# Performance work log

Measured on AMD Instinct MI355X. Metric: run time of the kernel, lower is better.

The kernel has to match this reference:

```python
import jax, jax.numpy as jnp
import numpy as np
import math

DIM = 256
D_STATE = 16
D_CONV = 4
EXPAND = 2
D_INNER = EXPAND * DIM
DT_RANK = math.ceil(DIM / 16)
B_, H_, W_ = 2, 48, 48


def setup_inputs() -> dict:
    key = jax.random.key(0)
    ks = jax.random.split(key, 13)
    s = lambda *sh: 1.0 / np.sqrt(sh[-1])
    inp = {
        "x": jax.random.normal(ks[0], (B_, DIM, H_, W_), jnp.float32),
        "ln_w": jnp.ones((DIM,), jnp.float32),
        "ln_b": jnp.zeros((DIM,), jnp.float32),
        "in_proj_w": jax.random.normal(ks[1], (2 * D_INNER, DIM), jnp.float32) * s(DIM),
        "conv_w": jax.random.normal(ks[2], (D_INNER, 1, D_CONV), jnp.float32) * s(D_CONV),
        "conv_b": jax.random.normal(ks[3], (D_INNER,), jnp.float32) * 0.1,
        "x_proj_w": jax.random.normal(ks[4], (DT_RANK + 2 * D_STATE, D_INNER), jnp.float32) * s(D_INNER),
        "dt_proj_w": jax.random.normal(ks[5], (D_INNER, DT_RANK), jnp.float32) * s(DT_RANK),
        "dt_proj_b": jax.random.uniform(ks[6], (D_INNER,), jnp.float32, -4.0, -1.0),  # softplus -> small dt
        "A_log": jnp.log(jnp.broadcast_to(jnp.arange(1, D_STATE + 1, dtype=jnp.float32), (D_INNER, D_STATE))),
        "D": jnp.ones((D_INNER,), jnp.float32),
        "out_proj_w": jax.random.normal(ks[7], (DIM, D_INNER), jnp.float32) * s(D_INNER),
        "gamma": jax.random.normal(ks[8], (1,), jnp.float32) * 0.1,
    }
    return inp


def _mamba(seq, in_proj_w, conv_w, conv_b, x_proj_w, dt_proj_w, dt_proj_b, A_log, D, out_proj_w):
    # seq: [B, L, dim]
    B, L, _ = seq.shape
    xz = seq @ in_proj_w.T                       # [B, L, 2*d_inner]
    x_in, z = jnp.split(xz, 2, axis=-1)
    # depthwise causal conv over time
    xt = jnp.transpose(x_in, (0, 2, 1))          # [B, d_inner, L]
    xc = jax.lax.conv_general_dilated(
        xt, conv_w, window_strides=(1,), padding=[(D_CONV - 1, 0)],
        feature_group_count=D_INNER, dimension_numbers=("NCH", "OIH", "NCH"))
    xc = xc + conv_b[None, :, None]
    xc = jax.nn.silu(xc)
    xu = jnp.transpose(xc, (0, 2, 1))            # [B, L, d_inner]
    # input-dependent SSM params
    x_dbl = xu @ x_proj_w.T                      # [B, L, dt_rank + 2N]
    dt, Bm, Cm = jnp.split(x_dbl, [DT_RANK, DT_RANK + D_STATE], axis=-1)
    delta = jax.nn.softplus(dt @ dt_proj_w.T + dt_proj_b)   # [B, L, d_inner]
    A = -jnp.exp(A_log)                          # [d_inner, N]
    dA = jnp.exp(delta[..., None] * A)           # [B, L, d_inner, N]
    dBx = (delta * xu)[..., None] * Bm[:, :, None, :]        # [B, L, d_inner, N]

    def step(h, ins):
        dA_t, dBx_t, C_t = ins
        h = dA_t * h + dBx_t                     # [B, d_inner, N]
        y = jnp.einsum("bdn,bn->bd", h, C_t)
        return h, y

    h0 = jnp.zeros((B, D_INNER, D_STATE), seq.dtype)
    xs = (jnp.swapaxes(dA, 0, 1), jnp.swapaxes(dBx, 0, 1), jnp.swapaxes(Cm, 0, 1))
    _, ys = jax.lax.scan(step, h0, xs)           # ys: [L, B, d_inner]
    y = jnp.swapaxes(ys, 0, 1) + xu * D          # [B, L, d_inner]
    y = y * jax.nn.silu(z)
    return y @ out_proj_w.T                      # [B, L, dim]


def reference(x, ln_w, ln_b, in_proj_w, conv_w, conv_b, x_proj_w, dt_proj_w,
              dt_proj_b, A_log, D, out_proj_w, gamma):
    B, C, H, W = x.shape
    shortcut = x
    xp = jnp.transpose(x, (0, 2, 3, 1))          # [B, H, W, C]
    mu = jnp.mean(xp, axis=-1, keepdims=True)
    var = jnp.var(xp, axis=-1, keepdims=True)
    xn = (xp - mu) * jax.lax.rsqrt(var + 1e-5) * ln_w + ln_b
    seq = xn.reshape(B, H * W, C)
    y = _mamba(seq, in_proj_w, conv_w, conv_b, x_proj_w, dt_proj_w, dt_proj_b,
               A_log, D, out_proj_w)
    y = jnp.transpose(y.reshape(B, H, W, C), (0, 3, 1, 2))
    return shortcut + gamma * y
```

## Files before the change

kernel.cpp:

```cpp
#include <hip/hip_runtime.h>
#include <math.h>

#define DIMC 256
#define DST 16
#define DIN 512
#define BB 2
#define HH 48
#define WW 48
#define LL (HH*WW)
#define MM (BB*LL)
#define CH 24
#define NC 96
#define NGRP (BB*DIN)
#define NSEQ (NGRP*DST)

typedef unsigned short ushort_t;
typedef __attribute__((ext_vector_type(8))) short bf16x8;
typedef __attribute__((ext_vector_type(4))) float f32x4;

__device__ __forceinline__ float silu_f(float a){ return a / (1.f + expf(-a)); }
__device__ __forceinline__ float softplus_f(float a){ return a > 20.f ? a : log1pf(__expf(a)); }
__device__ __forceinline__ ushort_t f2bf(float f) {
    unsigned u = __float_as_uint(f);
    u += 0x7FFFu + ((u >> 16) & 1u);
    return (ushort_t)(u >> 16);
}
__device__ __forceinline__ float bf2f(ushort_t h) {
    return __uint_as_float(((unsigned)h) << 16);
}

__global__ __launch_bounds__(256) void ln_kernel(const float* __restrict__ x,
    const float* __restrict__ w, const float* __restrict__ bgain,
    ushort_t* __restrict__ xn) {
    int pos = blockIdx.x;
    int b = pos / LL, l = pos % LL;
    int c = threadIdx.x;
    float v = x[((size_t)b*DIMC + c)*LL + l];
    float s = v, s2 = v*v;
    #pragma unroll
    for (int o = 32; o; o >>= 1) { s += __shfl_down(s, o); s2 += __shfl_down(s2, o); }
    __shared__ float ss[4], ss2[4];
    int wid = c >> 6;
    if ((c & 63) == 0) { ss[wid] = s; ss2[wid] = s2; }
    __syncthreads();
    float tot  = ss[0]+ss[1]+ss[2]+ss[3];
    float tot2 = ss2[0]+ss2[1]+ss2[2]+ss2[3];
    float mu = tot * (1.f/DIMC);
    float var = tot2 * (1.f/DIMC) - mu*mu;
    float r = rsqrtf(var + 1e-5f);
    xn[(size_t)pos*DIMC + c] = f2bf((v - mu)*r*w[c] + bgain[c]);
}

#define W0N (1024*256)
#define W1N (48*512)
#define W2N (256*512)
__global__ __launch_bounds__(256) void wconv_kernel(const float* __restrict__ w0,
    const float* __restrict__ w1, const float* __restrict__ w2,
    ushort_t* __restrict__ o0, ushort_t* __restrict__ o1, ushort_t* __restrict__ o2) {
    int i = blockIdx.x * 256 + threadIdx.x;
    if (i < W0N) o0[i] = f2bf(w0[i]);
    else if (i < W0N + W1N) o1[i - W0N] = f2bf(w1[i - W0N]);
    else o2[i - W0N - W1N] = f2bf(w2[i - W0N - W1N]);
}

template<int EPI>
__global__ __launch_bounds__(256) void mfma_gemm(const ushort_t* __restrict__ A,
    const ushort_t* __restrict__ W, float* __restrict__ C, int M, int N, int K,
    const float* __restrict__ Xres, const float* __restrict__ gammap,
    float* __restrict__ Out) {
    __shared__ ushort_t Asl[64][72];
    __shared__ ushort_t Bsl[64][72];
    int tid = threadIdx.x;
    int bm = blockIdx.y * 64;
    int bn = blockIdx.x * 64;
    int w = tid >> 6, l = tid & 63;
    int wr = (w >> 1) * 32, wc = (w & 1) * 32;
    int fr = l & 15, fg = l >> 4;
    f32x4 acc[2][2] = {};
    for (int k0 = 0; k0 < K; k0 += 64) {
        #pragma unroll
        for (int s = 0; s < 2; s++) {
            int c = tid + s*256;
            int r = c >> 3, c8 = (c & 7) * 8;
            *(uint4*)&Asl[r][c8] = *(const uint4*)(A + (size_t)(bm + r)*K + k0 + c8);
            uint4 wv = make_uint4(0u,0u,0u,0u);
            if (bn + r < N) wv = *(const uint4*)(W + (size_t)(bn + r)*K + k0 + c8);
            *(uint4*)&Bsl[r][c8] = wv;
        }
        __syncthreads();
        #pragma unroll
        for (int kk = 0; kk < 2; kk++) {
            int ko = kk*32 + fg*8;
            bf16x8 a0 = *(const bf16x8*)&Asl[wr + fr][ko];
            bf16x8 a1 = *(const bf16x8*)&Asl[wr + 16 + fr][ko];
            bf16x8 b0 = *(const bf16x8*)&Bsl[wc + fr][ko];
            bf16x8 b1 = *(const bf16x8*)&Bsl[wc + 16 + fr][ko];
            acc[0][0] = __builtin_amdgcn_mfma_f32_16x16x32_bf16(a0, b0, acc[0][0], 0,0,0);
            acc[0][1] = __builtin_amdgcn_mfma_f32_16x16x32_bf16(a0, b1, acc[0][1], 0,0,0);
            acc[1][0] = __builtin_amdgcn_mfma_f32_16x16x32_bf16(a1, b0, acc[1][0], 0,0,0);
            acc[1][1] = __builtin_amdgcn_mfma_f32_16x16x32_bf16(a1, b1, acc[1][1], 0,0,0);
        }
        __syncthreads();
    }
    if (EPI == 0) {
        #pragma unroll
        for (int mi = 0; mi < 2; mi++)
            #pragma unroll
            for (int nj = 0; nj < 2; nj++) {
                int n = bn + wc + nj*16 + fr;
                if (n < N) {
                    int mbase = bm + wr + mi*16 + fg*4;
                    #pragma unroll
                    for (int i = 0; i < 4; i++)
                        C[(size_t)(mbase + i)*N + n] = acc[mi][nj][i];
                }
            }
    } else {
        float g = gammap[0];
        int b = (bm >= LL) ? 1 : 0;
        #pragma unroll
        for (int mi = 0; mi < 2; mi++)
            #pragma unroll
            for (int nj = 0; nj < 2; nj++) {
                int n = bn + wc + nj*16 + fr;
                int mbase = bm + wr + mi*16 + fg*4;
                #pragma unroll
                for (int i = 0; i < 4; i++) {
                    size_t o = ((size_t)(b*DIMC + n))*LL + (size_t)(mbase + i - b*LL);
                    Out[o] = fmaf(g, acc[mi][nj][i], Xres[o]);
                }
            }
    }
}

__global__ __launch_bounds__(256) void conv_kernel(const float* __restrict__ xz,
    const float* __restrict__ cw, const float* __restrict__ cb,
    ushort_t* __restrict__ xu) {
    int idx = blockIdx.x * 256 + threadIdx.x;
    int d = idx & (DIN-1);
    int ml = idx >> 9;
    int l = ml % LL;
    float acc = cb[d];
    #pragma unroll
    for (int j = 0; j < 4; j++) {
        int ll = l - 3 + j;
        if (ll >= 0) acc = fmaf(cw[d*4 + j], xz[(size_t)(ml - l + ll)*1024 + d], acc);
    }
    xu[(size_t)ml*DIN + d] = f2bf(silu_f(acc));
}

#define LOAD16(arr, p) { float4 q0=(p)[0],q1=(p)[1],q2=(p)[2],q3=(p)[3]; \
    arr[0]=q0.x;arr[1]=q0.y;arr[2]=q0.z;arr[3]=q0.w; arr[4]=q1.x;arr[5]=q1.y;arr[6]=q1.z;arr[7]=q1.w; \
    arr[8]=q2.x;arr[9]=q2.y;arr[10]=q2.z;arr[11]=q2.w; arr[12]=q3.x;arr[13]=q3.y;arr[14]=q3.z;arr[15]=q3.w; }

__global__ __launch_bounds__(256) void scan_phase1(
    const ushort_t* __restrict__ xu, const float* __restrict__ xdbl,
    const float* __restrict__ dtw, const float* __restrict__ dtb,
    const float* __restrict__ A_log,
    float* __restrict__ aprod, float* __restrict__ hend) {
    int t = blockIdx.x * 256 + threadIdx.x;
    int g = t & (NGRP-1);
    int c = t >> 10;
    int b = g >> 9, d = g & (DIN-1);
    float dw[16], A[16], h[16], a[16];
    LOAD16(dw, (const float4*)(dtw + (size_t)d*16));
    #pragma unroll
    for (int n = 0; n < 16; n++) A[n] = -__expf(A_log[d*DST + n]);
    #pragma unroll
    for (int n = 0; n < 16; n++) { h[n] = 0.f; a[n] = 1.f; }
    float bias = dtb[d];
    int m0 = b*LL + c*CH;
    for (int l = 0; l < CH; l++) {
        int m = m0 + l;
        const float4* xr = (const float4*)(xdbl + (size_t)m*48);
        float4 t0 = xr[0], t1 = xr[1], t2 = xr[2], t3 = xr[3];
        float dlt = bias;
        dlt=fmaf(t0.x,dw[0],dlt); dlt=fmaf(t0.y,dw[1],dlt); dlt=fmaf(t0.z,dw[2],dlt); dlt=fmaf(t0.w,dw[3],dlt);
        dlt=fmaf(t1.x,dw[4],dlt); dlt=fmaf(t1.y,dw[5],dlt); dlt=fmaf(t1.z,dw[6],dlt); dlt=fmaf(t1.w,dw[7],dlt);
        dlt=fmaf(t2.x,dw[8],dlt); dlt=fmaf(t2.y,dw[9],dlt); dlt=fmaf(t2.z,dw[10],dlt); dlt=fmaf(t2.w,dw[11],dlt);
        dlt=fmaf(t3.x,dw[12],dlt); dlt=fmaf(t3.y,dw[13],dlt); dlt=fmaf(t3.z,dw[14],dlt); dlt=fmaf(t3.w,dw[15],dlt);
        dlt = softplus_f(dlt);
        float xv = bf2f(xu[(size_t)m*DIN + d]);
        float dbx = dlt * xv;
        float Bv[16];
        LOAD16(Bv, xr + 4);
        #pragma unroll
        for (int n = 0; n < 16; n++) {
            float dA = __expf(dlt * A[n]);
            h[n] = fmaf(dA, h[n], dbx * Bv[n]);
            a[n] *= dA;
        }
    }
    float4* ap = (float4*)(aprod + ((size_t)c*NGRP + g)*16);
    float4* hp = (float4*)(hend  + ((size_t)c*NGRP + g)*16);
    ap[0] = make_float4(a[0],a[1],a[2],a[3]);   ap[1] = make_float4(a[4],a[5],a[6],a[7]);
    ap[2] = make_float4(a[8],a[9],a[10],a[11]); ap[3] = make_float4(a[12],a[13],a[14],a[15]);
    hp[0] = make_float4(h[0],h[1],h[2],h[3]);   hp[1] = make_float4(h[4],h[5],h[6],h[7]);
    hp[2] = make_float4(h[8],h[9],h[10],h[11]); hp[3] = make_float4(h[12],h[13],h[14],h[15]);
}

__global__ __launch_bounds__(256) void scan_phase2(const float* __restrict__ aprod,
    const float* __restrict__ hend, float* __restrict__ hin) {
    int u = blockIdx.x * 256 + threadIdx.x;
    float h = 0.f;
    #pragma unroll 4
    for (int c = 0; c < NC; c++) {
        size_t ci = (size_t)c*NSEQ + u;
        hin[ci] = h;
        h = fmaf(aprod[ci], h, hend[ci]);
    }
}

__global__ __launch_bounds__(256) void scan_phase3(
    const ushort_t* __restrict__ xu, const float* __restrict__ xdbl,
    const float* __restrict__ dtw, const float* __restrict__ dtb,
    const float* __restrict__ A_log, const float* __restrict__ Dp,
    const float* __restrict__ xz, const float* __restrict__ hin,
    ushort_t* __restrict__ yg) {
    int t = blockIdx.x * 256 + threadIdx.x;
    int g = t & (NGRP-1);
    int c = t >> 10;
    int b = g >> 9, d = g & (DIN-1);
    float dw[16], A[16], h[16];
    LOAD16(dw, (const float4*)(dtw + (size_t)d*16));
    #pragma unroll
    for (int n = 0; n < 16; n++) A[n] = -__expf(A_log[d*DST + n]);
    LOAD16(h, (const float4*)(hin + ((size_t)c*NGRP + g)*16));
    float bias = dtb[d];
    float Dd = Dp[d];
    int m0 = b*LL + c*CH;
    for (int l = 0; l < CH; l++) {
        int m = m0 + l;
        const float4* xr = (const float4*)(xdbl + (size_t)m*48);
        float4 t0 = xr[0], t1 = xr[1], t2 = xr[2], t3 = xr[3];
        float dlt = bias;
        dlt=fmaf(t0.x,dw[0],dlt); dlt=fmaf(t0.y,dw[1],dlt); dlt=fmaf(t0.z,dw[2],dlt); dlt=fmaf(t0.w,dw[3],dlt);
        dlt=fmaf(t1.x,dw[4],dlt); dlt=fmaf(t1.y,dw[5],dlt); dlt=fmaf(t1.z,dw[6],dlt); dlt=fmaf(t1.w,dw[7],dlt);
        dlt=fmaf(t2.x,dw[8],dlt); dlt=fmaf(t2.y,dw[9],dlt); dlt=fmaf(t2.z,dw[10],dlt); dlt=fmaf(t2.w,dw[11],dlt);
        dlt=fmaf(t3.x,dw[12],dlt); dlt=fmaf(t3.y,dw[13],dlt); dlt=fmaf(t3.z,dw[14],dlt); dlt=fmaf(t3.w,dw[15],dlt);
        dlt = softplus_f(dlt);
        float xv = bf2f(xu[(size_t)m*DIN + d]);
        float dbx = dlt * xv;
        float Bv[16], Cv[16];
        LOAD16(Bv, xr + 4);
        LOAD16(Cv, xr + 8);
        float y = 0.f;
        #pragma unroll
        for (int n = 0; n < 16; n++) {
            float dA = __expf(dlt * A[n]);
            h[n] = fmaf(dA, h[n], dbx * Bv[n]);
            y = fmaf(h[n], Cv[n], y);
        }
        float z = xz[(size_t)m*1024 + 512 + d];
        float yv = fmaf(xv, Dd, y);
        yg[(size_t)m*DIN + d] = f2bf(yv * (z / (1.f + __expf(-z))));
    }
}

extern "C" void kernel_launch(void* const* d_in, const int* in_sizes, int n_in,
                              void* d_out, int out_size, void* d_ws, size_t ws_size,
                              hipStream_t stream) {
    const float* x         = (const float*)d_in[0];
    const float* ln_w      = (const float*)d_in[1];
    const float* ln_b      = (const float*)d_in[2];
    const float* in_proj_w = (const float*)d_in[3];
    const float* conv_w    = (const float*)d_in[4];
    const float* conv_b    = (const float*)d_in[5];
    const float* x_proj_w  = (const float*)d_in[6];
    const float* dt_proj_w = (const float*)d_in[7];
    const float* dt_proj_b = (const float*)d_in[8];
    const float* A_log     = (const float*)d_in[9];
    const float* Dp        = (const float*)d_in[10];
    const float* out_proj_w= (const float*)d_in[11];
    const float* gamma     = (const float*)d_in[12];
    float* out = (float*)d_out;

    float* ws = (float*)d_ws;
    float* xz    = ws;
    float* x_dbl = xz    + (size_t)MM*1024;
    float* aprod = x_dbl + (size_t)MM*48;
    float* hend  = aprod + (size_t)NC*NSEQ;
    float* hin   = hend  + (size_t)NC*NSEQ;
    ushort_t* xn  = (ushort_t*)(hin + (size_t)NC*NSEQ);
    ushort_t* xu  = xn  + (size_t)MM*DIMC;
    ushort_t* yg  = xu  + (size_t)MM*DIN;
    ushort_t* win = yg  + (size_t)MM*DIN;
    ushort_t* wxp = win + (size_t)W0N;
    ushort_t* wout= wxp + (size_t)W1N;

    ln_kernel<<<MM, 256, 0, stream>>>(x, ln_w, ln_b, xn);
    wconv_kernel<<<(W0N+W1N+W2N)/256, 256, 0, stream>>>(in_proj_w, x_proj_w, out_proj_w, win, wxp, wout);
    mfma_gemm<0><<<dim3(1024/64, MM/64), 256, 0, stream>>>(xn, win, xz, MM, 1024, DIMC, nullptr, nullptr, nullptr);
    conv_kernel<<<(MM*DIN)/256, 256, 0, stream>>>(xz, conv_w, conv_b, xu);
    mfma_gemm<0><<<dim3(1, MM/64), 256, 0, stream>>>(xu, wxp, x_dbl, MM, 48, DIN, nullptr, nullptr, nullptr);
    scan_phase1<<<(NC*NGRP)/256, 256, 0, stream>>>(xu, x_dbl, dt_proj_w, dt_proj_b, A_log, aprod, hend);
    scan_phase2<<<NSEQ/256, 256, 0, stream>>>(aprod, hend, hin);
    scan_phase3<<<(NC*NGRP)/256, 256, 0, stream>>>(xu, x_dbl, dt_proj_w, dt_proj_b, A_log, Dp, xz, hin, yg);
    mfma_gemm<2><<<dim3(DIMC/64, MM/64), 256, 0, stream>>>(yg, wout, nullptr, MM, DIMC, DIN, x, gamma, out);
}
```

Baseline: 212.4 us.

## Retile LayerNorm, split in-proj GEMM output, stage x_dbl in LDS, precompute A

LayerNorm now handles 16 positions per block and goes through an LDS transpose, so both the read and the bf16 write are coalesced. The in_proj GEMM uses 128x128 tiles and writes x as bf16 and z as fp32 into separate buffers, and the conv reads the bf16 x. The scan chunk is halved to 12 steps, giving twice as many chunks and more parallelism. The x_dbl rows are staged in shared memory per block, and -exp(A_log) is computed once in the weight-setup kernel. In exchange, phase 2 has more carry traffic, the in_proj output path adds bf16 rounding, and the larger GEMM tile uses more registers.

```diff
diff --git a/kernel.cpp b/kernel.cpp
--- a/kernel.cpp
+++ b/kernel.cpp
@@ -9,10 +9,11 @@
 #define WW 48
 #define LL (HH*WW)
 #define MM (BB*LL)
-#define CH 24
-#define NC 96
+#define CH 12
+#define NC 192
 #define NGRP (BB*DIN)
 #define NSEQ (NGRP*DST)
+#define LTILE 16
 
 typedef unsigned short ushort_t;
 typedef __attribute__((ext_vector_type(8))) short bf16x8;
@@ -32,35 +33,122 @@
 __global__ __launch_bounds__(256) void ln_kernel(const float* __restrict__ x,
     const float* __restrict__ w, const float* __restrict__ bgain,
     ushort_t* __restrict__ xn) {
-    int pos = blockIdx.x;
-    int b = pos / LL, l = pos % LL;
-    int c = threadIdx.x;
-    float v = x[((size_t)b*DIMC + c)*LL + l];
-    float s = v, s2 = v*v;
-    #pragma unroll
-    for (int o = 32; o; o >>= 1) { s += __shfl_down(s, o); s2 += __shfl_down(s2, o); }
-    __shared__ float ss[4], ss2[4];
-    int wid = c >> 6;
-    if ((c & 63) == 0) { ss[wid] = s; ss2[wid] = s2; }
-    __syncthreads();
-    float tot  = ss[0]+ss[1]+ss[2]+ss[3];
-    float tot2 = ss2[0]+ss2[1]+ss2[2]+ss2[3];
-    float mu = tot * (1.f/DIMC);
-    float var = tot2 * (1.f/DIMC) - mu*mu;
-    float r = rsqrtf(var + 1e-5f);
-    xn[(size_t)pos*DIMC + c] = f2bf((v - mu)*r*w[c] + bgain[c]);
+    __shared__ float T2[LTILE][DIMC + 4];
+    __shared__ float PS[16][17], PS2[16][17];
+    __shared__ float MUB[LTILE], RB[LTILE];
+    int blk = blockIdx.x;
+    int b = blk / (LL/LTILE);
+    int l0 = (blk % (LL/LTILE)) * LTILE;
+    int t = threadIdx.x;
+    int p = t & 15, g = t >> 4;
+    float v[16];
+    float s = 0.f, s2 = 0.f;
+    #pragma unroll
+    for (int cc = 0; cc < 16; cc++) {
+        int c = g*16 + cc;
+        float vv = x[((size_t)(b*DIMC + c))*LL + l0 + p];
+        v[cc] = vv;
+        s += vv; s2 += vv*vv;
+    }
+    PS[g][p] = s; PS2[g][p] = s2;
+    __syncthreads();
+    if (t < 16) {
+        float tot = 0.f, tot2 = 0.f;
+        #pragma unroll
+        for (int gg = 0; gg < 16; gg++) { tot += PS[gg][t]; tot2 += PS2[gg][t]; }
+        float mu = tot * (1.f/DIMC);
+        float var = tot2 * (1.f/DIMC) - mu*mu;
+        MUB[t] = mu;
+        RB[t] = rsqrtf(var + 1e-5f);
+    }
+    __syncthreads();
+    float mu = MUB[p], r = RB[p];
+    #pragma unroll
+    for (int cc = 0; cc < 16; cc++) {
+        int c = g*16 + cc;
+        T2[p][c] = (v[cc] - mu) * r * w[c] + bgain[c];
+    }
+    __syncthreads();
+    int c4 = (t & 63) * 4;
+    int prow = t >> 6;
+    #pragma unroll
+    for (int pp = 0; pp < 4; pp++) {
+        int pos = pp*4 + prow;
+        float4 q = *(const float4*)&T2[pos][c4];
+        ushort4 o;
+        o.x = f2bf(q.x); o.y = f2bf(q.y); o.z = f2bf(q.z); o.w = f2bf(q.w);
+        *(ushort4*)&xn[((size_t)(b*LL + l0 + pos))*DIMC + c4] = o;
+    }
 }
 
 #define W0N (1024*256)
 #define W1N (48*512)
 #define W2N (256*512)
-__global__ __launch_bounds__(256) void wconv_kernel(const float* __restrict__ w0,
+__global__ __launch_bounds__(256) void wsetup_kernel(const float* __restrict__ w0,
     const float* __restrict__ w1, const float* __restrict__ w2,
-    ushort_t* __restrict__ o0, ushort_t* __restrict__ o1, ushort_t* __restrict__ o2) {
+    const float* __restrict__ A_log,
+    ushort_t* __restrict__ o0, ushort_t* __restrict__ o1, ushort_t* __restrict__ o2,
+    float* __restrict__ A2) {
     int i = blockIdx.x * 256 + threadIdx.x;
     if (i < W0N) o0[i] = f2bf(w0[i]);
     else if (i < W0N + W1N) o1[i - W0N] = f2bf(w1[i - W0N]);
-    else o2[i - W0N - W1N] = f2bf(w2[i - W0N - W1N]);
+    else if (i < W0N + W1N + W2N) o2[i - W0N - W1N] = f2bf(w2[i - W0N - W1N]);
+    if (i < DIN*DST) A2[i] = -__expf(A_log[i]);
+}
+
+__global__ __launch_bounds__(256) void mfma_gemm128_split(const ushort_t* __restrict__ A,
+    const ushort_t* __restrict__ W, ushort_t* __restrict__ Xs, float* __restrict__ Zb,
+    int K) {
+    __shared__ ushort_t Asl[128][72];
+    __shared__ ushort_t Bsl[128][72];
+    int tid = threadIdx.x;
+    int bm = blockIdx.y * 128;
+    int bn = blockIdx.x * 128;
+    int w = tid >> 6, l = tid & 63;
+    int wr = (w >> 1) * 64, wc = (w & 1) * 64;
+    int fr = l & 15, fg = l >> 4;
+    f32x4 acc[4][4] = {};
+    for (int k0 = 0; k0 < K; k0 += 64) {
+        #pragma unroll
+        for (int s = 0; s < 4; s++) {
+            int c = tid + s*256;
+            int r = c >> 3, c8 = (c & 7) * 8;
+            *(uint4*)&Asl[r][c8] = *(const uint4*)(A + (size_t)(bm + r)*K + k0 + c8);
+            *(uint4*)&Bsl[r][c8] = *(const uint4*)(W + (size_t)(bn + r)*K + k0 + c8);
+        }
+        __syncthreads();
+        #pragma unroll
+        for (int kk = 0; kk < 2; kk++) {
+            int ko = kk*32 + fg*8;
+            bf16x8 af[4], bf[4];
+            #pragma unroll
+            for (int i = 0; i < 4; i++) af[i] = *(const bf16x8*)&Asl[wr + i*16 + fr][ko];
+            #pragma unroll
+            for (int j = 0; j < 4; j++) bf[j] = *(const bf16x8*)&Bsl[wc + j*16 + fr][ko];
+            #pragma unroll
+            for (int i = 0; i < 4; i++)
+                #pragma unroll
+                for (int j = 0; j < 4; j++)
+                    acc[i][j] = __builtin_amdgcn_mfma_f32_16x16x32_bf16(af[i], bf[j], acc[i][j], 0,0,0);
+        }
+        __syncthreads();
+    }
+    #pragma unroll
+    for (int i = 0; i < 4; i++)
+        #pragma unroll
+        for (int j = 0; j < 4; j++) {
+            int n = bn + wc + j*16 + fr;
+            int mbase = bm + wr + i*16 + fg*4;
+            if (n < DIN) {
+                #pragma unroll
+                for (int ii = 0; ii < 4; ii++)
+                    Xs[(size_t)(mbase+ii)*DIN + n] = f2bf(acc[i][j][ii]);
+            } else {
+                #pragma unroll
+                for (int ii = 0; ii < 4; ii++)
+                    Zb[(size_t)(mbase+ii)*DIN + (n - DIN)] = acc[i][j][ii];
+            }
+        }
 }
 
 template<int EPI>
@@ -133,7 +221,7 @@
     }
 }
 
-__global__ __launch_bounds__(256) void conv_kernel(const float* __restrict__ xz,
+__global__ __launch_bounds__(256) void conv_kernel(const ushort_t* __restrict__ xs,
     const float* __restrict__ cw, const float* __restrict__ cb,
     ushort_t* __restrict__ xu) {
     int idx = blockIdx.x * 256 + threadIdx.x;
@@ -144,7 +232,7 @@
     #pragma unroll
     for (int j = 0; j < 4; j++) {
         int ll = l - 3 + j;
-        if (ll >= 0) acc = fmaf(cw[d*4 + j], xz[(size_t)(ml - l + ll)*1024 + d], acc);
+        if (ll >= 0) acc = fmaf(cw[d*4 + j], bf2f(xs[(size_t)(ml - l + ll)*DIN + d]), acc);
     }
     xu[(size_t)ml*DIN + d] = f2bf(silu_f(acc));
 }
@@ -153,34 +241,37 @@
     arr[0]=q0.x;arr[1]=q0.y;arr[2]=q0.z;arr[3]=q0.w; arr[4]=q1.x;arr[5]=q1.y;arr[6]=q1.z;arr[7]=q1.w; \
     arr[8]=q2.x;arr[9]=q2.y;arr[10]=q2.z;arr[11]=q2.w; arr[12]=q3.x;arr[13]=q3.y;arr[14]=q3.z;arr[15]=q3.w; }
 
+#define DT_DOT(dlt, xr) { float4 t0 = (xr)[0], t1 = (xr)[1], t2 = (xr)[2], t3 = (xr)[3]; \
+    dlt=fmaf(t0.x,dw[0],dlt); dlt=fmaf(t0.y,dw[1],dlt); dlt=fmaf(t0.z,dw[2],dlt); dlt=fmaf(t0.w,dw[3],dlt); \
+    dlt=fmaf(t1.x,dw[4],dlt); dlt=fmaf(t1.y,dw[5],dlt); dlt=fmaf(t1.z,dw[6],dlt); dlt=fmaf(t1.w,dw[7],dlt); \
+    dlt=fmaf(t2.x,dw[8],dlt); dlt=fmaf(t2.y,dw[9],dlt); dlt=fmaf(t2.z,dw[10],dlt); dlt=fmaf(t2.w,dw[11],dlt); \
+    dlt=fmaf(t3.x,dw[12],dlt); dlt=fmaf(t3.y,dw[13],dlt); dlt=fmaf(t3.z,dw[14],dlt); dlt=fmaf(t3.w,dw[15],dlt); }
+
 __global__ __launch_bounds__(256) void scan_phase1(
     const ushort_t* __restrict__ xu, const float* __restrict__ xdbl,
     const float* __restrict__ dtw, const float* __restrict__ dtb,
-    const float* __restrict__ A_log,
+    const float* __restrict__ A2,
     float* __restrict__ aprod, float* __restrict__ hend) {
+    __shared__ float xs_s[CH*48];
     int t = blockIdx.x * 256 + threadIdx.x;
     int g = t & (NGRP-1);
     int c = t >> 10;
     int b = g >> 9, d = g & (DIN-1);
+    int m0 = b*LL + c*CH;
+    for (int i = threadIdx.x; i < CH*48; i += 256) xs_s[i] = xdbl[(size_t)m0*48 + i];
     float dw[16], A[16], h[16], a[16];
     LOAD16(dw, (const float4*)(dtw + (size_t)d*16));
-    #pragma unroll
-    for (int n = 0; n < 16; n++) A[n] = -__expf(A_log[d*DST + n]);
+    LOAD16(A,  (const float4*)(A2  + (size_t)d*16));
     #pragma unroll
     for (int n = 0; n < 16; n++) { h[n] = 0.f; a[n] = 1.f; }
     float bias = dtb[d];
-    int m0 = b*LL + c*CH;
+    __syncthreads();
     for (int l = 0; l < CH; l++) {
-        int m = m0 + l;
-        const float4* xr = (const float4*)(xdbl + (size_t)m*48);
-        float4 t0 = xr[0], t1 = xr[1], t2 = xr[2], t3 = xr[3];
+        const float4* xr = (const float4*)&xs_s[l*48];
         float dlt = bias;
-        dlt=fmaf(t0.x,dw[0],dlt); dlt=fmaf(t0.y,dw[1],dlt); dlt=fmaf(t0.z,dw[2],dlt); dlt=fmaf(t0.w,dw[3],dlt);
-        dlt=fmaf(t1.x,dw[4],dlt); dlt=fmaf(t1.y,dw[5],dlt); dlt=fmaf(t1.z,dw[6],dlt); dlt=fmaf(t1.w,dw[7],dlt);
-        dlt=fmaf(t2.x,dw[8],dlt); dlt=fmaf(t2.y,dw[9],dlt); dlt=fmaf(t2.z,dw[10],dlt); dlt=fmaf(t2.w,dw[11],dlt);
-        dlt=fmaf(t3.x,dw[12],dlt); dlt=fmaf(t3.y,dw[13],dlt); dlt=fmaf(t3.z,dw[14],dlt); dlt=fmaf(t3.w,dw[15],dlt);
+        DT_DOT(dlt, xr);
         dlt = softplus_f(dlt);
-        float xv = bf2f(xu[(size_t)m*DIN + d]);
+        float xv = bf2f(xu[(size_t)(m0 + l)*DIN + d]);
         float dbx = dlt * xv;
         float Bv[16];
         LOAD16(Bv, xr + 4);
@@ -214,30 +305,28 @@
 __global__ __launch_bounds__(256) void scan_phase3(
     const ushort_t* __restrict__ xu, const float* __restrict__ xdbl,
     const float* __restrict__ dtw, const float* __restrict__ dtb,
-    const float* __restrict__ A_log, const float* __restrict__ Dp,
-    const float* __restrict__ xz, const float* __restrict__ hin,
+    const float* __restrict__ A2, const float* __restrict__ Dp,
+    const float* __restrict__ zbuf, const float* __restrict__ hin,
     ushort_t* __restrict__ yg) {
+    __shared__ float xs_s[CH*48];
     int t = blockIdx.x * 256 + threadIdx.x;
     int g = t & (NGRP-1);
     int c = t >> 10;
     int b = g >> 9, d = g & (DIN-1);
+    int m0 = b*LL + c*CH;
+    for (int i = threadIdx.x; i < CH*48; i += 256) xs_s[i] = xdbl[(size_t)m0*48 + i];
     float dw[16], A[16], h[16];
     LOAD16(dw, (const float4*)(dtw + (size_t)d*16));
-    #pragma unroll
-    for (int n = 0; n < 16; n++) A[n] = -__expf(A_log[d*DST + n]);
-    LOAD16(h, (const float4*)(hin + ((size_t)c*NGRP + g)*16));
+    LOAD16(A,  (const float4*)(A2  + (size_t)d*16));
+    LOAD16(h,  (const float4*)(hin + ((size_t)c*NGRP + g)*16));
     float bias = dtb[d];
     float Dd = Dp[d];
-    int m0 = b*LL + c*CH;
+    __syncthreads();
     for (int l = 0; l < CH; l++) {
         int m = m0 + l;
-        const float4* xr = (const float4*)(xdbl + (size_t)m*48);
-        float4 t0 = xr[0], t1 = xr[1], t2 = xr[2], t3 = xr[3];
+        const float4* xr = (const float4*)&xs_s[l*48];
         float dlt = bias;
-        dlt=fmaf(t0.x,dw[0],dlt); dlt=fmaf(t0.y,dw[1],dlt); dlt=fmaf(t0.z,dw[2],dlt); dlt=fmaf(t0.w,dw[3],dlt);
-        dlt=fmaf(t1.x,dw[4],dlt); dlt=fmaf(t1.y,dw[5],dlt); dlt=fmaf(t1.z,dw[6],dlt); dlt=fmaf(t1.w,dw[7],dlt);
-        dlt=fmaf(t2.x,dw[8],dlt); dlt=fmaf(t2.y,dw[9],dlt); dlt=fmaf(t2.z,dw[10],dlt); dlt=fmaf(t2.w,dw[11],dlt);
-        dlt=fmaf(t3.x,dw[12],dlt); dlt=fmaf(t3.y,dw[13],dlt); dlt=fmaf(t3.z,dw[14],dlt); dlt=fmaf(t3.w,dw[15],dlt);
+        DT_DOT(dlt, xr);
         dlt = softplus_f(dlt);
         float xv = bf2f(xu[(size_t)m*DIN + d]);
         float dbx = dlt * xv;
@@ -251,7 +340,7 @@
             h[n] = fmaf(dA, h[n], dbx * Bv[n]);
             y = fmaf(h[n], Cv[n], y);
         }
-        float z = xz[(size_t)m*1024 + 512 + d];
+        float z = zbuf[(size_t)m*DIN + d];
         float yv = fmaf(xv, Dd, y);
         yg[(size_t)m*DIN + d] = f2bf(yv * (z / (1.f + __expf(-z))));
     }
@@ -276,25 +365,27 @@
     float* out = (float*)d_out;
 
     float* ws = (float*)d_ws;
-    float* xz    = ws;
-    float* x_dbl = xz    + (size_t)MM*1024;
+    float* zbuf  = ws;
+    float* x_dbl = zbuf  + (size_t)MM*DIN;
     float* aprod = x_dbl + (size_t)MM*48;
     float* hend  = aprod + (size_t)NC*NSEQ;
     float* hin   = hend  + (size_t)NC*NSEQ;
-    ushort_t* xn  = (ushort_t*)(hin + (size_t)NC*NSEQ);
-    ushort_t* xu  = xn  + (size_t)MM*DIMC;
+    float* A2    = hin   + (size_t)NC*NSEQ;
+    ushort_t* xn  = (ushort_t*)(A2 + DIN*DST);
+    ushort_t* xs  = xn  + (size_t)MM*DIMC;
+    ushort_t* xu  = xs  + (size_t)MM*DIN;
     ushort_t* yg  = xu  + (size_t)MM*DIN;
     ushort_t* win = yg  + (size_t)MM*DIN;
     ushort_t* wxp = win + (size_t)W0N;
     ushort_t* wout= wxp + (size_t)W1N;
 
-    ln_kernel<<<MM, 256, 0, stream>>>(x, ln_w, ln_b, xn);
-    wconv_kernel<<<(W0N+W1N+W2N)/256, 256, 0, stream>>>(in_proj_w, x_proj_w, out_proj_w, win, wxp, wout);
-    mfma_gemm<0><<<dim3(1024/64, MM/64), 256, 0, stream>>>(xn, win, xz, MM, 1024, DIMC, nullptr, nullptr, nullptr);
-    conv_kernel<<<(MM*DIN)/256, 256, 0, stream>>>(xz, conv_w, conv_b, xu);
+    ln_kernel<<<BB*(LL/LTILE), 256, 0, stream>>>(x, ln_w, ln_b, xn);
+    wsetup_kernel<<<(W0N+W1N+W2N+255)/256, 256, 0, stream>>>(in_proj_w, x_proj_w, out_proj_w, A_log, win, wxp, wout, A2);
+    mfma_gemm128_split<<<dim3(1024/128, MM/128), 256, 0, stream>>>(xn, win, xs, zbuf, DIMC);
+    conv_kernel<<<(MM*DIN)/256, 256, 0, stream>>>(xs, conv_w, conv_b, xu);
     mfma_gemm<0><<<dim3(1, MM/64), 256, 0, stream>>>(xu, wxp, x_dbl, MM, 48, DIN, nullptr, nullptr, nullptr);
-    scan_phase1<<<(NC*NGRP)/256, 256, 0, stream>>>(xu, x_dbl, dt_proj_w, dt_proj_b, A_log, aprod, hend);
+    scan_phase1<<<(NC*NGRP)/256, 256, 0, stream>>>(xu, x_dbl, dt_proj_w, dt_proj_b, A2, aprod, hend);
     scan_phase2<<<NSEQ/256, 256, 0, stream>>>(aprod, hend, hin);
-    scan_phase3<<<(NC*NGRP)/256, 256, 0, stream>>>(xu, x_dbl, dt_proj_w, dt_proj_b, A_log, Dp, xz, hin, yg);
+    scan_phase3<<<(NC*NGRP)/256, 256, 0, stream>>>(xu, x_dbl, dt_proj_w, dt_proj_b, A2, Dp, zbuf, hin, yg);
     mfma_gemm<2><<<dim3(DIMC/64, MM/64), 256, 0, stream>>>(yg, wout, nullptr, MM, DIMC, DIN, x, gamma, out);
 }
```

Result: faster. 202.5 us (-4.7%).
